# Performance work log

Measured on AMD Instinct MI355X. Metric: run time of the kernel, lower is better.

Reference implementation:

```python
import jax, jax.numpy as jnp
import numpy as np

N, E, G = 20000, 320000, 16
IN, HID, OUT, HEADS = 256, 64, 256, 4
D0 = HID * HEADS  # 256, output dim of layer 0 (concat)


def _p(key, shape, scale=0.05):
    return (jax.random.normal(key, shape, dtype=jnp.float32) * scale)


def setup_inputs() -> dict:
    key = jax.random.key(0)
    ks = jax.random.split(key, 24)
    x = jax.random.normal(ks[0], (N, IN), dtype=jnp.float32)
    edge_index = jax.random.randint(ks[1], (2, E), 0, N, dtype=jnp.int64)
    batch = jnp.sort(jax.random.randint(ks[2], (N,), 0, G, dtype=jnp.int64))
    d = {"x": x, "edge_index": edge_index, "batch": batch}
    # Layer 0: TransformerConv(256 -> 64, heads=4, concat=True, beta=True)
    d["Wq0"] = _p(ks[3], (IN, D0)); d["bq0"] = jnp.zeros((D0,), jnp.float32)
    d["Wk0"] = _p(ks[4], (IN, D0)); d["bk0"] = jnp.zeros((D0,), jnp.float32)
    d["Wv0"] = _p(ks[5], (IN, D0)); d["bv0"] = jnp.zeros((D0,), jnp.float32)
    d["Ws0"] = _p(ks[6], (IN, D0)); d["bs0"] = jnp.zeros((D0,), jnp.float32)
    d["Wb0"] = _p(ks[7], (3 * D0, 1))
    d["g0"] = jnp.ones((D0,), jnp.float32); d["b0"] = jnp.zeros((D0,), jnp.float32)
    # Layer 1: TransformerConv(256 -> 256, heads=1, concat=False, beta=True)
    d["Wq1"] = _p(ks[8], (D0, OUT)); d["bq1"] = jnp.zeros((OUT,), jnp.float32)
    d["Wk1"] = _p(ks[9], (D0, OUT)); d["bk1"] = jnp.zeros((OUT,), jnp.float32)
    d["Wv1"] = _p(ks[10], (D0, OUT)); d["bv1"] = jnp.zeros((OUT,), jnp.float32)
    d["Ws1"] = _p(ks[11], (D0, OUT)); d["bs1"] = jnp.zeros((OUT,), jnp.float32)
    d["Wb1"] = _p(ks[12], (3 * OUT, 1))
    d["g1"] = jnp.ones((OUT,), jnp.float32); d["b1"] = jnp.zeros((OUT,), jnp.float32)
    return d


def _transformer_conv(x, src, dst, Wq, bq, Wk, bk, Wv, bv, Ws, bs, Wb, H, C, concat):
    n = x.shape[0]
    q = (x @ Wq + bq).reshape(n, H, C)
    k = (x @ Wk + bk).reshape(n, H, C)
    v = (x @ Wv + bv).reshape(n, H, C)
    # per-edge attention logits [E, H]
    alpha = (q[dst] * k[src]).sum(-1) / jnp.sqrt(jnp.asarray(C, jnp.float32))
    # segment softmax over incoming edges of each dst node
    m = jax.ops.segment_max(alpha, dst, num_segments=n)  # [N, H]
    a = jnp.exp(alpha - m[dst])
    s = jax.ops.segment_sum(a, dst, num_segments=n)  # [N, H]
    a = a / s[dst]
    out = jax.ops.segment_sum(a[:, :, None] * v[src], dst, num_segments=n)  # [N,H,C]
    out = out.reshape(n, H * C) if concat else out.mean(axis=1)
    # beta-gated skip connection
    r = x @ Ws + bs
    g = jax.nn.sigmoid(jnp.concatenate([out, r, out - r], axis=-1) @ Wb)  # [N,1]
    return g * r + (1.0 - g) * out


def _layer_norm(x, g, b, eps=1e-5):
    mu = x.mean(-1, keepdims=True)
    var = x.var(-1, keepdims=True)
    return (x - mu) * jax.lax.rsqrt(var + eps) * g + b


def reference(x, edge_index, batch,
              Wq0, bq0, Wk0, bk0, Wv0, bv0, Ws0, bs0, Wb0, g0, b0,
              Wq1, bq1, Wk1, bk1, Wv1, bv1, Ws1, bs1, Wb1, g1, b1):
    src, dst = edge_index[0], edge_index[1]
    h = _transformer_conv(x, src, dst, Wq0, bq0, Wk0, bk0, Wv0, bv0, Ws0, bs0, Wb0, HEADS, HID, True)
    h = jax.nn.relu(_layer_norm(h, g0, b0))  # dropout is identity at inference
    h = _transformer_conv(h, src, dst, Wq1, bq1, Wk1, bk1, Wv1, bv1, Ws1, bs1, Wb1, 1, OUT, False)
    h = _layer_norm(h, g1, b1)
    # global mean pool over graphs
    sums = jax.ops.segment_sum(h, batch, num_segments=G)
    counts = jax.ops.segment_sum(jnp.ones((h.shape[0],), h.dtype), batch, num_segments=G)
    return sums / jnp.maximum(counts, 1.0)[:, None]
```

## Files before the change

kernel.cpp:

```cpp
#include <hip/hip_runtime.h>
#include <hip/hip_bf16.h>


#define DEVFN static __device__ __forceinline__

typedef __attribute__((ext_vector_type(4))) float f32x4;
typedef __attribute__((ext_vector_type(2))) float f32x2;
typedef __attribute__((ext_vector_type(8))) short bf16x8;

#define GLOAD16(g, lds) __builtin_amdgcn_global_load_lds(                      \
    (const __attribute__((address_space(1))) unsigned int*)(g),                \
    (__attribute__((address_space(3))) unsigned int*)(lds), 16, 0, 0)

DEVFN float bfu2f(unsigned short u) {
    union { unsigned int i; float f; } t; t.i = ((unsigned)u) << 16; return t.f;
}
DEVFN unsigned short f2bu(float f) {
    __hip_bfloat16 b = __float2bfloat16(f);
    return __builtin_bit_cast(unsigned short, b);
}
DEVFN void stb4(__hip_bfloat16* p, float4 v) {
    ushort4 u;
    u.x = f2bu(v.x); u.y = f2bu(v.y); u.z = f2bu(v.z); u.w = f2bu(v.w);
    *reinterpret_cast<ushort4*>(p) = u;
}
DEVFN float4 f8x4_to_f4(unsigned u) {
    const f32x2 lo = __builtin_amdgcn_cvt_pk_f32_fp8((int)u, false);
    const f32x2 hi = __builtin_amdgcn_cvt_pk_f32_fp8((int)u, true);
    return make_float4(lo.x, lo.y, hi.x, hi.y);
}

DEVFN float dot16(const float* q, uint4 u) {
    const float4 f0 = f8x4_to_f4(u.x);
    const float4 f1 = f8x4_to_f4(u.y);
    const float4 f2 = f8x4_to_f4(u.z);
    const float4 f3 = f8x4_to_f4(u.w);
    float p;
    p = q[0] * f0.x;            p = fmaf(q[1],  f0.y, p);
    p = fmaf(q[2],  f0.z, p);   p = fmaf(q[3],  f0.w, p);
    p = fmaf(q[4],  f1.x, p);   p = fmaf(q[5],  f1.y, p);
    p = fmaf(q[6],  f1.z, p);   p = fmaf(q[7],  f1.w, p);
    p = fmaf(q[8],  f2.x, p);   p = fmaf(q[9],  f2.y, p);
    p = fmaf(q[10], f2.z, p);   p = fmaf(q[11], f2.w, p);
    p = fmaf(q[12], f3.x, p);   p = fmaf(q[13], f3.y, p);
    p = fmaf(q[14], f3.z, p);   p = fmaf(q[15], f3.w, p);
    return p;
}
DEVFN void accum16(float* acc, uint4 u, float a) {
    const float4 f0 = f8x4_to_f4(u.x);
    const float4 f1 = f8x4_to_f4(u.y);
    const float4 f2 = f8x4_to_f4(u.z);
    const float4 f3 = f8x4_to_f4(u.w);
    acc[0]  = fmaf(a, f0.x, acc[0]);  acc[1]  = fmaf(a, f0.y, acc[1]);
    acc[2]  = fmaf(a, f0.z, acc[2]);  acc[3]  = fmaf(a, f0.w, acc[3]);
    acc[4]  = fmaf(a, f1.x, acc[4]);  acc[5]  = fmaf(a, f1.y, acc[5]);
    acc[6]  = fmaf(a, f1.z, acc[6]);  acc[7]  = fmaf(a, f1.w, acc[7]);
    acc[8]  = fmaf(a, f2.x, acc[8]);  acc[9]  = fmaf(a, f2.y, acc[9]);
    acc[10] = fmaf(a, f2.z, acc[10]); acc[11] = fmaf(a, f2.w, acc[11]);
    acc[12] = fmaf(a, f3.x, acc[12]); acc[13] = fmaf(a, f3.y, acc[13]);
    acc[14] = fmaf(a, f3.z, acc[14]); acc[15] = fmaf(a, f3.w, acc[15]);
}

__global__ __launch_bounds__(256)
void prep_kernel(const float* __restrict__ x, __hip_bfloat16* __restrict__ xb, int nf2b,
                 const float* __restrict__ W0, const float* __restrict__ W1,
                 const float* __restrict__ W2, const float* __restrict__ W3,
                 const float* __restrict__ W4, const float* __restrict__ W5,
                 const float* __restrict__ W6, const float* __restrict__ W7,
                 __hip_bfloat16* __restrict__ Wt,
                 int4* __restrict__ zbase, int nz4)
{
    const int b = blockIdx.x;
    if (b < nf2b) {
        const int i = b * 256 + threadIdx.x;
        const float4 v = *reinterpret_cast<const float4*>(x + (size_t)i * 4);
        stb4(xb + (size_t)i * 4, v);
    } else if (b < nf2b + 2048) {
        const int wb = b - nf2b;
        const int z  = wb >> 8;
        const int k  = wb & 255;
        const int c  = threadIdx.x;
        const float* W;
        switch (z) {
            case 0: W = W0; break; case 1: W = W1; break;
            case 2: W = W2; break; case 3: W = W3; break;
            case 4: W = W4; break; case 5: W = W5; break;
            case 6: W = W6; break; default: W = W7; break;
        }
        Wt[(size_t)z * 65536 + (size_t)c * 256 + k] =
            __float2bfloat16(W[(size_t)k * 256 + c]);
    } else {
        const int i = (b - nf2b - 2048) * 256 + threadIdx.x;
        if (i < nz4) zbase[i] = make_int4(0, 0, 0, 0);
    }
}

#define SWZ64(r, kb) ((r) * 128 + ((kb) ^ (((r) & 7) << 4)))
#define TSTRIDE 272

__global__ __launch_bounds__(256)
void gemm_mfma_kernel(const __hip_bfloat16* __restrict__ A, int M,
                      const __hip_bfloat16* __restrict__ Wt,
                      const float* __restrict__ b0, const float* __restrict__ b1,
                      const float* __restrict__ b2, const float* __restrict__ b3,
                      void* __restrict__ O0, void* __restrict__ O1,
                      void* __restrict__ O2, void* __restrict__ O3,
                      int s0, int s1, int s2, int s3,
                      int f0, int f1, int f2, int f3)
{
    const int q8   = gridDim.x >> 3;
    const int wgid = (blockIdx.x & 7) * q8 + (blockIdx.x >> 3);
    const int rowblk = wgid >> 3;
    const int rem    = wgid & 7;
    const int colblk = rem >> 2;
    const int z      = rem & 3;

    const float* bias; void* O; int rs, isf8;
    switch (z) {
        case 0:  bias = b0; O = O0; rs = s0; isf8 = f0; break;
        case 1:  bias = b1; O = O1; rs = s1; isf8 = f1; break;
        case 2:  bias = b2; O = O2; rs = s2; isf8 = f2; break;
        default: bias = b3; O = O3; rs = s3; isf8 = f3; break;
    }
    const __hip_bfloat16* Wz = Wt + (size_t)z * 65536;

    __shared__ __align__(16) char Sh[128 * TSTRIDE];
    char* As = Sh;
    char* Bs = Sh + 16384;

    const int tid  = threadIdx.x;
    const int row0 = rowblk * 128;
    const int col0 = colblk * 128;
    const int wid  = tid >> 6, lane = tid & 63;
    const int wr   = wid >> 1, wc = wid & 1;
    const int lrow = lane & 15, kg = lane >> 4;

    f32x4 acc[4][4] = {};

    for (int k0 = 0; k0 < 256; k0 += 64) {
        #pragma unroll
        for (int j = 0; j < 4; ++j) {
            const int s_lin = j * 4096 + wid * 1024 + lane * 16;
            const int r     = s_lin >> 7;
            const int kb    = (s_lin & 127) ^ ((r & 7) << 4);
            const int kelem = k0 + (kb >> 1);
            char* ldsA = As + j * 4096 + wid * 1024;
            char* ldsB = Bs + j * 4096 + wid * 1024;
            const int gr = row0 + r;
            if (gr < M)
                GLOAD16(A + (size_t)gr * 256 + kelem, ldsA);
            GLOAD16(Wz + (size_t)(col0 + r) * 256 + kelem, ldsB);
        }
        __syncthreads();

        #pragma unroll
        for (int kk = 0; kk < 64; kk += 32) {
            const int kbyte = kk * 2 + kg * 16;
            bf16x8 af[4], bfr[4];
            #pragma unroll
            for (int m = 0; m < 4; ++m) {
                const int r = wr * 64 + m * 16 + lrow;
                af[m] = *reinterpret_cast<const bf16x8*>(As + SWZ64(r, kbyte));
            }
            #pragma unroll
            for (int n = 0; n < 4; ++n) {
                const int c = wc * 64 + n * 16 + lrow;
                bfr[n] = *reinterpret_cast<const bf16x8*>(Bs + SWZ64(c, kbyte));
            }
            #pragma unroll
            for (int m = 0; m < 4; ++m)
                #pragma unroll
                for (int n = 0; n < 4; ++n)
                    acc[m][n] = __builtin_amdgcn_mfma_f32_16x16x32_bf16(
                        af[m], bfr[n], acc[m][n], 0, 0, 0);
        }
        __syncthreads();
    }

    #pragma unroll
    for (int m = 0; m < 4; ++m) {
        #pragma unroll
        for (int j = 0; j < 4; ++j) {
            const int rr = wr * 64 + m * 16 + kg * 4 + j;
            #pragma unroll
            for (int n = 0; n < 4; ++n) {
                const int cc = wc * 64 + n * 16 + lrow;
                const float v = acc[m][n][j] + bias[col0 + cc];
                *reinterpret_cast<unsigned short*>(Sh + rr * TSTRIDE + cc * 2) = f2bu(v);
            }
        }
    }
    __syncthreads();

    const int row  = tid >> 1;
    const int half = tid & 1;
    const int grow = row0 + row;
    if (grow >= M) return;
    const char* src = Sh + row * TSTRIDE + half * 128;

    if (isf8) {
        unsigned char* dst = (unsigned char*)O + (size_t)grow * rs + col0 + half * 64;
        #pragma unroll
        for (int i2 = 0; i2 < 4; ++i2) {
            uint4 w;
            unsigned tmp[4];
            #pragma unroll
            for (int c8 = 0; c8 < 2; ++c8) {
                const bf16x8 e = *reinterpret_cast<const bf16x8*>(src + (i2 * 2 + c8) * 16);
                const int p0 = __builtin_amdgcn_cvt_pk_fp8_f32(
                    bfu2f((unsigned short)e[0]), bfu2f((unsigned short)e[1]), 0, false);
                const int p1 = __builtin_amdgcn_cvt_pk_fp8_f32(
                    bfu2f((unsigned short)e[2]), bfu2f((unsigned short)e[3]), 0, false);
                const int p2 = __builtin_amdgcn_cvt_pk_fp8_f32(
                    bfu2f((unsigned short)e[4]), bfu2f((unsigned short)e[5]), 0, false);
                const int p3 = __builtin_amdgcn_cvt_pk_fp8_f32(
                    bfu2f((unsigned short)e[6]), bfu2f((unsigned short)e[7]), 0, false);
                tmp[c8 * 2 + 0] = (unsigned)(p0 & 0xFFFF) | ((unsigned)(p1 & 0xFFFF) << 16);
                tmp[c8 * 2 + 1] = (unsigned)(p2 & 0xFFFF) | ((unsigned)(p3 & 0xFFFF) << 16);
            }
            w.x = tmp[0]; w.y = tmp[1]; w.z = tmp[2]; w.w = tmp[3];
            *reinterpret_cast<uint4*>(dst + i2 * 16) = w;
        }
    } else {
        char* dst = (char*)((__hip_bfloat16*)O + (size_t)grow * rs + col0 + half * 64);
        #pragma unroll
        for (int i = 0; i < 8; ++i)
            *reinterpret_cast<ulonglong2*>(dst + i * 16) =
                *reinterpret_cast<const ulonglong2*>(src + i * 16);
    }
}

__global__ __launch_bounds__(256)
void build_kernel(const int* __restrict__ ei, int E, int* __restrict__ deg, int nhist,
                  const int* __restrict__ batch, int N, int* __restrict__ gcount)
{
    if (blockIdx.x < nhist) {
        const int e = blockIdx.x * 256 + threadIdx.x;
        if (e < E) atomicAdd(&deg[ei[E + e]], 1);
    } else {
        __shared__ int h[16];
        if (threadIdx.x < 16) h[threadIdx.x] = 0;
        __syncthreads();
        const int n = (blockIdx.x - nhist) * 256 + threadIdx.x;
        if (n < N) atomicAdd(&h[batch[n]], 1);
        __syncthreads();
        if (threadIdx.x < 16 && h[threadIdx.x] != 0)
            atomicAdd(&gcount[threadIdx.x], h[threadIdx.x]);
    }
}

__global__ __launch_bounds__(1024)
void scan_kernel(const int* __restrict__ deg, int* __restrict__ row_start, int n,
                 const int* __restrict__ gcount, int* __restrict__ gstart)
{
    __shared__ int wsum[16];
    __shared__ int wincl[16];
    const int tid  = threadIdx.x;
    const int w    = tid >> 6;
    const int lane = tid & 63;
    if (tid == 0) {
        row_start[0] = 0;
        int o = 0;
        #pragma unroll
        for (int g = 0; g < 16; ++g) { gstart[g] = o; o += gcount[g]; }
        gstart[16] = o;
    }
    int offset = 0;
    for (int base = 0; base < n; base += 1024) {
        const int idx = base + tid;
        int s = (idx < n) ? deg[idx] : 0;
        #pragma unroll
        for (int d = 1; d < 64; d <<= 1) {
            const int t = __shfl_up(s, d, 64);
            if (lane >= d) s += t;
        }
        if (lane == 63) wsum[w] = s;
        __syncthreads();
        if (tid < 16) {
            int si = wsum[tid];
            #pragma unroll
            for (int d = 1; d < 16; d <<= 1) {
                const int u = __shfl_up(si, d, 64);
                if (tid >= d) si += u;
            }
            wincl[tid] = si;
        }
        __syncthreads();
        const int woff = (w > 0) ? wincl[w - 1] : 0;
        if (idx < n) row_start[idx + 1] = offset + woff + s;
        offset += wincl[15];
        __syncthreads();
    }
}

__global__ __launch_bounds__(256)
void fill_kernel(const int* __restrict__ ei, int E,
                 const int* __restrict__ row_start,
                 int* __restrict__ cursor, int* __restrict__ csr_src)
{
    const int e = blockIdx.x * 256 + threadIdx.x;
    if (e >= E) return;
    const int s = ei[e];
    const int d = ei[E + e];
    const int pos = atomicAdd(&cursor[d], 1);
    csr_src[row_start[d] + pos] = s;
}

template <int NSH, bool RELU, bool OUTB>
__global__ __launch_bounds__(128)
void attn_kernel(const __hip_bfloat16* __restrict__ Q,
                 const unsigned char* __restrict__ KV,
                 const __hip_bfloat16* __restrict__ R,
                 const float* __restrict__ Wb, const float* __restrict__ lng,
                 const float* __restrict__ lnb,
                 const int* __restrict__ row_start, const int* __restrict__ csr_src,
                 __hip_bfloat16* __restrict__ outb, float* __restrict__ outf,
                 int N, float scale)
{
    const int wv   = threadIdx.x >> 6;
    const int lane = threadIdx.x & 63;
    const int g    = lane >> 4;
    const int s    = lane & 15;
    const int node = blockIdx.x * 2 + wv;
    if (node >= N) return;

    float q[16];
    {
        const bf16x8 a = *reinterpret_cast<const bf16x8*>(Q + (size_t)node * 256 + s * 16);
        const bf16x8 b = *reinterpret_cast<const bf16x8*>(Q + (size_t)node * 256 + s * 16 + 8);
        #pragma unroll
        for (int j = 0; j < 8; ++j) {
            q[j]     = bfu2f((unsigned short)a[j]);
            q[8 + j] = bfu2f((unsigned short)b[j]);
        }
    }

    const int beg = row_start[node];
    const int end = row_start[node + 1];

    float acc[16] = {};
    float ssum = 0.f;

    int i = beg + g;
    for (; i + 4 < end; i += 8) {
        const int sa = csr_src[i];
        const int sb = csr_src[i + 4];
        const uint4 ka = *reinterpret_cast<const uint4*>(KV + (size_t)sa * 512 + s * 16);
        const uint4 va = *reinterpret_cast<const uint4*>(KV + (size_t)sa * 512 + 256 + s * 16);
        const uint4 kb = *reinterpret_cast<const uint4*>(KV + (size_t)sb * 512 + s * 16);
        const uint4 vb = *reinterpret_cast<const uint4*>(KV + (size_t)sb * 512 + 256 + s * 16);
        float pa = dot16(q, ka);
        float pb = dot16(q, kb);
        #pragma unroll
        for (int m = 1; m < (1 << NSH); m <<= 1) {
            pa += __shfl_xor(pa, m, 64);
            pb += __shfl_xor(pb, m, 64);
        }
        const float aa = __expf(pa * scale);
        const float ab = __expf(pb * scale);
        ssum += aa + ab;
        accum16(acc, va, aa);
        accum16(acc, vb, ab);
    }
    if (i < end) {
        const int sa = csr_src[i];
        const uint4 ka = *reinterpret_cast<const uint4*>(KV + (size_t)sa * 512 + s * 16);
        const uint4 va = *reinterpret_cast<const uint4*>(KV + (size_t)sa * 512 + 256 + s * 16);
        float pa = dot16(q, ka);
        #pragma unroll
        for (int m = 1; m < (1 << NSH); m <<= 1) pa += __shfl_xor(pa, m, 64);
        const float aa = __expf(pa * scale);
        ssum += aa;
        accum16(acc, va, aa);
    }

    ssum += __shfl_xor(ssum, 16, 64);
    ssum += __shfl_xor(ssum, 32, 64);
    #pragma unroll
    for (int j = 0; j < 16; ++j) {
        acc[j] += __shfl_xor(acc[j], 16, 64);
        acc[j] += __shfl_xor(acc[j], 32, 64);
    }

    if (g != 0) return;

    const float is = (ssum > 0.f) ? 1.f / ssum : 0.f;
    float o[16];
    #pragma unroll
    for (int j = 0; j < 16; ++j) o[j] = acc[j] * is;

    float r[16];
    {
        const bf16x8 a = *reinterpret_cast<const bf16x8*>(R + (size_t)node * 256 + s * 16);
        const bf16x8 b = *reinterpret_cast<const bf16x8*>(R + (size_t)node * 256 + s * 16 + 8);
        #pragma unroll
        for (int j = 0; j < 8; ++j) {
            r[j]     = bfu2f((unsigned short)a[j]);
            r[8 + j] = bfu2f((unsigned short)b[j]);
        }
    }

    float z = 0.f;
    #pragma unroll
    for (int j = 0; j < 16; ++j) {
        const int d = s * 16 + j;
        z += o[j] * Wb[d] + r[j] * Wb[256 + d] + (o[j] - r[j]) * Wb[512 + d];
    }
    #pragma unroll
    for (int m = 1; m < 16; m <<= 1) z += __shfl_xor(z, m, 64);
    const float gg = 1.f / (1.f + __expf(-z));

    float h[16];
    float s1 = 0.f, s2 = 0.f;
    #pragma unroll
    for (int j = 0; j < 16; ++j) {
        h[j] = gg * r[j] + (1.f - gg) * o[j];
        s1 += h[j];
        s2 += h[j] * h[j];
    }
    #pragma unroll
    for (int m = 1; m < 16; m <<= 1) {
        s1 += __shfl_xor(s1, m, 64);
        s2 += __shfl_xor(s2, m, 64);
    }
    const float mu  = s1 * (1.f / 256.f);
    const float var = s2 * (1.f / 256.f) - mu * mu;
    const float inv = rsqrtf(var + 1e-5f);

    #pragma unroll
    for (int j = 0; j < 16; ++j) {
        const int d = s * 16 + j;
        h[j] = (h[j] - mu) * inv * lng[d] + lnb[d];
        if (RELU) h[j] = fmaxf(h[j], 0.f);
    }

    if (OUTB) {
        __hip_bfloat16* dst = outb + (size_t)node * 256 + s * 16;
        stb4(dst,      make_float4(h[0],  h[1],  h[2],  h[3]));
        stb4(dst + 4,  make_float4(h[4],  h[5],  h[6],  h[7]));
        stb4(dst + 8,  make_float4(h[8],  h[9],  h[10], h[11]));
        stb4(dst + 12, make_float4(h[12], h[13], h[14], h[15]));
    } else {
        float* dst = outf + (size_t)node * 256 + s * 16;
        #pragma unroll
        for (int c4 = 0; c4 < 4; ++c4)
            *reinterpret_cast<float4*>(dst + c4 * 4) =
                make_float4(h[c4 * 4], h[c4 * 4 + 1], h[c4 * 4 + 2], h[c4 * 4 + 3]);
    }
}

__global__ __launch_bounds__(256)
void pool_partial_kernel(const float* __restrict__ h, const int* __restrict__ gstart,
                         float* __restrict__ partial)
{
    const int s    = blockIdx.x;
    const int g    = blockIdx.y;
    const int tid  = threadIdx.x;
    const int quad = tid & 63;
    const int sub  = tid >> 6;

    const int beg = gstart[g];
    const int cnt = gstart[g + 1] - beg;

    f32x4 acc = {0.f, 0.f, 0.f, 0.f};
    for (int i = s * 4 + sub; i < cnt; i += 64) {
        const f32x4 v = *reinterpret_cast<const f32x4*>(
            h + (size_t)(beg + i) * 256 + quad * 4);
        acc += v;
    }

    __shared__ f32x4 sh[4][64];
    sh[sub][quad] = acc;
    __syncthreads();
    if (sub == 0) {
        const f32x4 r = sh[0][quad] + sh[1][quad] + sh[2][quad] + sh[3][quad];
        *reinterpret_cast<f32x4*>(partial + ((size_t)(g * 16 + s) * 64 + quad) * 4) = r;
    }
}

__global__ __launch_bounds__(256)
void pool_final_kernel(const float* __restrict__ partial, const int* __restrict__ gcount,
                       float* __restrict__ out)
{
    const int g = blockIdx.x;
    const int d = threadIdx.x;
    float sum = 0.f;
    #pragma unroll
    for (int s = 0; s < 16; ++s)
        sum += partial[(size_t)(g * 16 + s) * 256 + d];
    out[(size_t)g * 256 + d] = sum / (float)max(gcount[g], 1);
}

extern "C" void kernel_launch(void* const* d_in, const int* in_sizes, int n_in,
                              void* d_out, int out_size, void* d_ws, size_t ws_size,
                              hipStream_t stream)
{
    const float* x     = (const float*)d_in[0];
    const int*   ei    = (const int*)d_in[1];
    const int*   batch = (const int*)d_in[2];
    const float* Wq0 = (const float*)d_in[3];  const float* bq0 = (const float*)d_in[4];
    const float* Wk0 = (const float*)d_in[5];  const float* bk0 = (const float*)d_in[6];
    const float* Wv0 = (const float*)d_in[7];  const float* bv0 = (const float*)d_in[8];
    const float* Ws0 = (const float*)d_in[9];  const float* bs0 = (const float*)d_in[10];
    const float* Wb0 = (const float*)d_in[11];
    const float* g0  = (const float*)d_in[12]; const float* b0  = (const float*)d_in[13];
    const float* Wq1 = (const float*)d_in[14]; const float* bq1 = (const float*)d_in[15];
    const float* Wk1 = (const float*)d_in[16]; const float* bk1 = (const float*)d_in[17];
    const float* Wv1 = (const float*)d_in[18]; const float* bv1 = (const float*)d_in[19];
    const float* Ws1 = (const float*)d_in[20]; const float* bs1 = (const float*)d_in[21];
    const float* Wb1 = (const float*)d_in[22];
    const float* g1  = (const float*)d_in[23]; const float* b1  = (const float*)d_in[24];

    const int N = in_sizes[0] / 256;
    const int E = in_sizes[1] / 2;
    const int G = 16;
    const size_t NM = (size_t)N * 256;

    __hip_bfloat16* bws = (__hip_bfloat16*)d_ws;
    __hip_bfloat16* xb  = bws;
    __hip_bfloat16* qb  = xb  + NM;
    __hip_bfloat16* rb  = qb  + NM;
    __hip_bfloat16* h0b = rb  + NM;
    __hip_bfloat16* wt  = h0b + NM;
    unsigned char* kvb  = (unsigned char*)(wt + 8 * 65536);
    float* h1f     = (float*)(kvb + (size_t)N * 512);
    float* partial = h1f + NM;
    int* deg       = (int*)(partial + 16 * 16 * 256);
    int* row_start = deg + N;
    int* cursor    = row_start + N + 1;
    int* gcount    = cursor + N;
    int* gstart    = gcount + G;
    int* csr_src   = gstart + 17;

    const int eb = (E + 255) / 256;
    const int nb = (N + 255) / 256;
    const int nf2b = (int)((NM / 4 + 255) / 256);

    const int zwords = 3 * N + G + 18;
    const int nz4    = (zwords + 3) / 4;
    const int nzb    = (nz4 + 255) / 256;

    prep_kernel<<<nf2b + 2048 + nzb, 256, 0, stream>>>(x, xb, nf2b,
        Wq0, Wk0, Wv0, Ws0, Wq1, Wk1, Wv1, Ws1, wt,
        (int4*)deg, nz4);

    build_kernel<<<eb + nb, 256, 0, stream>>>(ei, E, deg, eb, batch, N, gcount);
    scan_kernel<<<1, 1024, 0, stream>>>(deg, row_start, N, gcount, gstart);
    fill_kernel<<<eb, 256, 0, stream>>>(ei, E, row_start, cursor, csr_src);

    const int nrb   = (N + 127) / 128;
    const int ggrid = nrb * 8;
    const int agrid = (N + 1) / 2;

    gemm_mfma_kernel<<<ggrid, 256, 0, stream>>>(xb, N, wt,
        bq0, bk0, bv0, bs0,
        qb, kvb, kvb + 256, rb,
        256, 512, 512, 256,
        0, 1, 1, 0);
    attn_kernel<2, true, true><<<agrid, 128, 0, stream>>>(
        qb, kvb, rb, Wb0, g0, b0, row_start, csr_src, h0b, nullptr, N, 0.125f);

    gemm_mfma_kernel<<<ggrid, 256, 0, stream>>>(h0b, N, wt + 4 * 65536,
        bq1, bk1, bv1, bs1,
        qb, kvb, kvb + 256, rb,
        256, 512, 512, 256,
        0, 1, 1, 0);
    attn_kernel<4, false, false><<<agrid, 128, 0, stream>>>(
        qb, kvb, rb, Wb1, g1, b1, row_start, csr_src, nullptr, h1f, N, 0.0625f);

    pool_partial_kernel<<<dim3(16, 16), 256, 0, stream>>>(h1f, gstart, partial);
    pool_final_kernel<<<16, 256, 0, stream>>>(partial, gcount, (float*)d_out);
}
```

Measured before the change: 202.6 us.

## Double-buffer GEMM K-loop and fuse CSR fill into first GEMM launch

The GEMM K-loop now uses two LDS buffers, so the global-to-LDS load of the next 64-wide K slice is issued before computing on the current one, with explicit vmcnt waits and raw barriers in place of __syncthreads. The separate CSR fill kernel is removed and its work runs as extra trailing blocks of the first GEMM launch, which saves one launch and lets the fill overlap GEMM work. Out-of-range rows are now clamped to M-1 instead of skipped. LDS per block grows to 64 KB, which may lower occupancy.

Result: faster. 195.6 us (-3.5%).

```diff
diff --git a/kernel.cpp b/kernel.cpp
--- a/kernel.cpp
+++ b/kernel.cpp
@@ -106,10 +106,27 @@
                       void* __restrict__ O0, void* __restrict__ O1,
                       void* __restrict__ O2, void* __restrict__ O3,
                       int s0, int s1, int s2, int s3,
-                      int f0, int f1, int f2, int f3)
-{
-    const int q8   = gridDim.x >> 3;
-    const int wgid = (blockIdx.x & 7) * q8 + (blockIdx.x >> 3);
+                      int f0, int f1, int f2, int f3,
+                      int ngemm,
+                      const int* __restrict__ ei, int E, int efill,
+                      const int* __restrict__ row_start,
+                      int* __restrict__ cursor, int* __restrict__ csr_src)
+{
+    __shared__ __align__(16) char Sh[65536];
+
+    if ((int)blockIdx.x >= ngemm) {
+        const int e = ((int)blockIdx.x - ngemm) * 256 + threadIdx.x;
+        if (e < efill) {
+            const int s = ei[e];
+            const int d = ei[E + e];
+            const int pos = atomicAdd(&cursor[d], 1);
+            csr_src[row_start[d] + pos] = s;
+        }
+        return;
+    }
+
+    const int q8   = ngemm >> 3;
+    const int wgid = ((int)blockIdx.x & 7) * q8 + ((int)blockIdx.x >> 3);
     const int rowblk = wgid >> 3;
     const int rem    = wgid & 7;
     const int colblk = rem >> 2;
@@ -124,9 +141,8 @@
     }
     const __hip_bfloat16* Wz = Wt + (size_t)z * 65536;
 
-    __shared__ __align__(16) char Sh[128 * TSTRIDE];
-    char* As = Sh;
-    char* Bs = Sh + 16384;
+    char* AsB[2] = {Sh,         Sh + 32768};
+    char* BsB[2] = {Sh + 16384, Sh + 49152};
 
     const int tid  = threadIdx.x;
     const int row0 = rowblk * 128;
@@ -137,22 +153,39 @@
 
     f32x4 acc[4][4] = {};
 
-    for (int k0 = 0; k0 < 256; k0 += 64) {
-        #pragma unroll
-        for (int j = 0; j < 4; ++j) {
-            const int s_lin = j * 4096 + wid * 1024 + lane * 16;
-            const int r     = s_lin >> 7;
-            const int kb    = (s_lin & 127) ^ ((r & 7) << 4);
-            const int kelem = k0 + (kb >> 1);
-            char* ldsA = As + j * 4096 + wid * 1024;
-            char* ldsB = Bs + j * 4096 + wid * 1024;
-            const int gr = row0 + r;
-            if (gr < M)
-                GLOAD16(A + (size_t)gr * 256 + kelem, ldsA);
-            GLOAD16(Wz + (size_t)(col0 + r) * 256 + kelem, ldsB);
-        }
-        __syncthreads();
-
+#define STAGE(buf, k0)                                                        \
+    {                                                                         \
+        _Pragma("unroll")                                                     \
+        for (int j = 0; j < 4; ++j) {                                         \
+            const int s_lin = j * 4096 + wid * 1024 + lane * 16;              \
+            const int r     = s_lin >> 7;                                     \
+            const int kb    = (s_lin & 127) ^ ((r & 7) << 4);                 \
+            const int kelem = (k0) + (kb >> 1);                               \
+            char* ldsA = AsB[buf] + j * 4096 + wid * 1024;                    \
+            char* ldsB = BsB[buf] + j * 4096 + wid * 1024;                    \
+            const int gr = min(row0 + r, M - 1);                              \
+            GLOAD16(A + (size_t)gr * 256 + kelem, ldsA);                      \
+            GLOAD16(Wz + (size_t)(col0 + r) * 256 + kelem, ldsB);             \
+        }                                                                     \
+    }
+
+    STAGE(0, 0);
+
+    #pragma unroll
+    for (int t = 0; t < 4; ++t) {
+        const int cur = t & 1;
+        if (t < 3) {
+            STAGE(cur ^ 1, (t + 1) * 64);
+            asm volatile("s_waitcnt vmcnt(8)" ::: "memory");
+        } else {
+            asm volatile("s_waitcnt vmcnt(0)" ::: "memory");
+        }
+        __builtin_amdgcn_sched_barrier(0);
+        __builtin_amdgcn_s_barrier();
+        __builtin_amdgcn_sched_barrier(0);
+
+        const char* As = AsB[cur];
+        const char* Bs = BsB[cur];
         #pragma unroll
         for (int kk = 0; kk < 64; kk += 32) {
             const int kbyte = kk * 2 + kg * 16;
@@ -174,8 +207,12 @@
                     acc[m][n] = __builtin_amdgcn_mfma_f32_16x16x32_bf16(
                         af[m], bfr[n], acc[m][n], 0, 0, 0);
         }
-        __syncthreads();
-    }
+        asm volatile("s_waitcnt lgkmcnt(0)" ::: "memory");
+        __builtin_amdgcn_sched_barrier(0);
+        __builtin_amdgcn_s_barrier();
+        __builtin_amdgcn_sched_barrier(0);
+    }
+#undef STAGE
 
     #pragma unroll
     for (int m = 0; m < 4; ++m) {
@@ -293,19 +330,6 @@
     }
 }
 
-__global__ __launch_bounds__(256)
-void fill_kernel(const int* __restrict__ ei, int E,
-                 const int* __restrict__ row_start,
-                 int* __restrict__ cursor, int* __restrict__ csr_src)
-{
-    const int e = blockIdx.x * 256 + threadIdx.x;
-    if (e >= E) return;
-    const int s = ei[e];
-    const int d = ei[E + e];
-    const int pos = atomicAdd(&cursor[d], 1);
-    csr_src[row_start[d] + pos] = s;
-}
-
 template <int NSH, bool RELU, bool OUTB>
 __global__ __launch_bounds__(128)
 void attn_kernel(const __hip_bfloat16* __restrict__ Q,
@@ -546,25 +570,26 @@
 
     build_kernel<<<eb + nb, 256, 0, stream>>>(ei, E, deg, eb, batch, N, gcount);
     scan_kernel<<<1, 1024, 0, stream>>>(deg, row_start, N, gcount, gstart);
-    fill_kernel<<<eb, 256, 0, stream>>>(ei, E, row_start, cursor, csr_src);
 
     const int nrb   = (N + 127) / 128;
-    const int ggrid = nrb * 8;
+    const int ngemm = nrb * 8;
     const int agrid = (N + 1) / 2;
 
-    gemm_mfma_kernel<<<ggrid, 256, 0, stream>>>(xb, N, wt,
+    gemm_mfma_kernel<<<ngemm + eb, 256, 0, stream>>>(xb, N, wt,
         bq0, bk0, bv0, bs0,
         qb, kvb, kvb + 256, rb,
         256, 512, 512, 256,
-        0, 1, 1, 0);
+        0, 1, 1, 0,
+        ngemm, ei, E, E, row_start, cursor, csr_src);
     attn_kernel<2, true, true><<<agrid, 128, 0, stream>>>(
         qb, kvb, rb, Wb0, g0, b0, row_start, csr_src, h0b, nullptr, N, 0.125f);
 
-    gemm_mfma_kernel<<<ggrid, 256, 0, stream>>>(h0b, N, wt + 4 * 65536,
+    gemm_mfma_kernel<<<ngemm, 256, 0, stream>>>(h0b, N, wt + 4 * 65536,
         bq1, bk1, bv1, bs1,
         qb, kvb, kvb + 256, rb,
         256, 512, 512, 256,
-        0, 1, 1, 0);
+        0, 1, 1, 0,
+        ngemm, ei, E, 0, row_start, cursor, csr_src);
     attn_kernel<4, false, false><<<agrid, 128, 0, stream>>>(
         qb, kvb, rb, Wb1, g1, b1, row_start, csr_src, nullptr, h1f, N, 0.0625f);
 
```
